# Optimization experiments

Hardware: AMD Instinct MI355X
Metric: run time of the kernel (lower is better)

The kernel has to match this reference:

```python
import jax, jax.numpy as jnp
import numpy as np

B, T, V = 32, 100, 20000
E, H, M, DD = 128, 128, 64, 2


def setup_inputs() -> dict:
    key = jax.random.key(0)
    ks = jax.random.split(key, 12)
    x = jax.random.uniform(ks[0], (B, T, V), dtype=jnp.float32)
    # zero out trailing timesteps per example so Masking layer matters
    lens = jax.random.randint(ks[1], (B,), T * 3 // 4, T + 1)
    tmask = (jnp.arange(T)[None, :] < lens[:, None]).astype(jnp.float32)
    x = x * tmask[:, :, None]
    a = jax.random.uniform(ks[2], (B, V), dtype=jnp.float32)
    d = jax.random.normal(ks[3], (B, DD), dtype=jnp.float32)
    # parameters
    emb = jax.random.uniform(ks[4], (V, E), minval=-0.1, maxval=0.1, dtype=jnp.float32)
    s = 1.0 / np.sqrt(E)
    gru_k = jax.random.uniform(ks[5], (E, 3 * H), minval=-s, maxval=s, dtype=jnp.float32)
    gru_rk = jax.random.normal(ks[6], (H, 3 * H), dtype=jnp.float32) / np.sqrt(H)
    gru_b_i = jnp.zeros((3 * H,), jnp.float32)   # input bias (reset_after=True)
    gru_b_r = jnp.zeros((3 * H,), jnp.float32)   # recurrent bias
    s1 = 1.0 / np.sqrt(H + E)
    W1 = jax.random.uniform(ks[7], (H + E, M), minval=-s1, maxval=s1, dtype=jnp.float32)
    b1 = jnp.zeros((M,), jnp.float32)
    s2 = 1.0 / np.sqrt(M + DD)
    W2 = jax.random.uniform(ks[8], (M + DD, 1), minval=-s2, maxval=s2, dtype=jnp.float32)
    b2 = jnp.zeros((1,), jnp.float32)
    return dict(x=x, a=a, d=d, emb=emb, gru_k=gru_k, gru_rk=gru_rk,
                gru_b_i=gru_b_i, gru_b_r=gru_b_r, W1=W1, b1=b1, W2=W2, b2=b2)


def _gru_final_state(xe, mask, gru_k, gru_rk, gru_b_i, gru_b_r):
    # xe: [B,T,E], mask: [B,T] bool. Keras GRU, reset_after=True, eval mode (dropout off).
    Hn = gru_rk.shape[0]
    x_proj = jnp.einsum('bte,eh->bth', xe, gru_k) + gru_b_i  # [B,T,3H]

    def step(h, inp):
        xp_t, m_t = inp                      # [B,3H], [B]
        rec = h @ gru_rk + gru_b_r           # [B,3H]
        xz, xr, xh = jnp.split(xp_t, 3, axis=-1)
        rz, rr, rh = jnp.split(rec, 3, axis=-1)
        z = jax.nn.sigmoid(xz + rz)
        r = jax.nn.sigmoid(xr + rr)
        hh = jnp.tanh(xh + r * rh)
        h_new = z * h + (1.0 - z) * hh
        h = jnp.where(m_t[:, None], h_new, h)  # masked steps carry state
        return h, None

    h0 = jnp.zeros((xe.shape[0], Hn), xe.dtype)
    h_final, _ = jax.lax.scan(step, h0, (jnp.swapaxes(x_proj, 0, 1), jnp.swapaxes(mask, 0, 1)))
    return h_final


def reference(x, a, d, emb, gru_k, gru_rk, gru_b_i, gru_b_r, W1, b1, W2, b2):
    ae = jnp.tanh(a @ emb)                       # [B,E]
    xe = jnp.tanh(jnp.einsum('btv,ve->bte', x, emb))  # [B,T,E]
    mask = jnp.any(xe != 0.0, axis=-1)           # Masking(mask_value=0.0)
    h = _gru_final_state(xe, mask, gru_k, gru_rk, gru_b_i, gru_b_r)  # [B,H]
    c = jnp.tanh(jnp.concatenate([h, ae], axis=1) @ W1 + b1)         # [B,M]
    out = jax.nn.sigmoid(jnp.concatenate([c, d], axis=1) @ W2 + b2)  # [B,1]
    return out
```

## Files before the change

### kernel.cpp

```cpp
#include <hip/hip_runtime.h>

typedef __attribute__((ext_vector_type(8))) short short8;
typedef __attribute__((ext_vector_type(4))) float float4v;

#define V_ 20000
#define KS 8
#define MPAD 3328

__device__ __forceinline__ unsigned short f2bf(float f) {
    union { float f; unsigned int u; } v; v.f = f;
    unsigned int u = v.u;
    u += 0x7fffu + ((u >> 16) & 1u);
    return (unsigned short)(u >> 16);
}

__device__ __forceinline__ float fast_tanh(float x) {
    float xc = fminf(15.f, fmaxf(-15.f, x));
    float e = __expf(2.f * xc);
    return (e - 1.f) / (e + 1.f);
}

__device__ __forceinline__ float sigmoidf_(float x) {
    float xc = fminf(30.f, fmaxf(-30.f, x));
    return 1.f / (1.f + __expf(-xc));
}

__global__ __launch_bounds__(256) void cvt_embT(const float* __restrict__ emb,
                                                unsigned short* __restrict__ embT) {
    __shared__ unsigned short tile[128 * 65];
    int tid = threadIdx.x;
    int k0 = blockIdx.x * 64;
    const float4v* e4 = (const float4v*)emb;
    #pragma unroll
    for (int c = 0; c < 8; ++c) {
        int l4 = c * 256 + tid;
        int k = l4 >> 5;
        int n4 = l4 & 31;
        float4v f = {0.f, 0.f, 0.f, 0.f};
        if (k0 + k < V_) f = e4[(size_t)(k0 + k) * 32 + n4];
        tile[(n4 * 4 + 0) * 65 + k] = f2bf(f.x);
        tile[(n4 * 4 + 1) * 65 + k] = f2bf(f.y);
        tile[(n4 * 4 + 2) * 65 + k] = f2bf(f.z);
        tile[(n4 * 4 + 3) * 65 + k] = f2bf(f.w);
    }
    __syncthreads();
    #pragma unroll
    for (int c = 0; c < 4; ++c) {
        int l8 = c * 256 + tid;
        int n = l8 >> 3, seg = l8 & 7;
        int kk = k0 + seg * 8;
        if (kk < V_) {
            short8 v;
            #pragma unroll
            for (int i = 0; i < 8; ++i) v[i] = (short)tile[n * 65 + seg * 8 + i];
            *(short8*)(embT + (size_t)n * V_ + kk) = v;
        }
    }
}

__global__ __launch_bounds__(256) void big_gemm(const float* __restrict__ x,
                                                const float* __restrict__ a,
                                                const unsigned short* __restrict__ embT,
                                                float* __restrict__ partial) {
    __shared__ unsigned short Alds[128 * 40];
    __shared__ unsigned short Blds[128 * 40];
    int tid = threadIdx.x;
    int bx = blockIdx.x, by = blockIdx.y;
    int m0 = bx * 128;
    const int per = 625 / KS, extra = 625 % KS;
    int kb0 = by * per + (by < extra ? by : extra);
    int nkb = per + (by < extra ? 1 : 0);

    int lane = tid & 63, wave = tid >> 6;
    int wr = wave >> 1, wc = wave & 1;
    int ln = lane & 15, quad = lane >> 4;

    float4v acc[4][4];
    #pragma unroll
    for (int i = 0; i < 4; ++i)
        #pragma unroll
        for (int j = 0; j < 4; ++j) acc[i][j] = (float4v){0.f, 0.f, 0.f, 0.f};

    int row = tid >> 1, seg = tid & 1;
    int rg = m0 + row;
    int aidx = rg - 3200; if (aidx < 0) aidx = 0; if (aidx > 31) aidx = 31;
    const float* __restrict__ srcA = (rg < 3200) ? (x + (size_t)rg * V_)
                                                 : (a + (size_t)aidx * V_);
    const unsigned short* __restrict__ srcB = embT + (size_t)row * V_;

    for (int it = 0; it < nkb; ++it) {
        int k0 = (kb0 + it) * 32;
        const float4v* ap = (const float4v*)(srcA + k0 + seg * 16);
        float4v f0 = ap[0], f1 = ap[1], f2 = ap[2], f3 = ap[3];
        short8 w0, w1;
        w0[0]=(short)f2bf(f0.x); w0[1]=(short)f2bf(f0.y); w0[2]=(short)f2bf(f0.z); w0[3]=(short)f2bf(f0.w);
        w0[4]=(short)f2bf(f1.x); w0[5]=(short)f2bf(f1.y); w0[6]=(short)f2bf(f1.z); w0[7]=(short)f2bf(f1.w);
        w1[0]=(short)f2bf(f2.x); w1[1]=(short)f2bf(f2.y); w1[2]=(short)f2bf(f2.z); w1[3]=(short)f2bf(f2.w);
        w1[4]=(short)f2bf(f3.x); w1[5]=(short)f2bf(f3.y); w1[6]=(short)f2bf(f3.z); w1[7]=(short)f2bf(f3.w);
        *(short8*)&Alds[row * 40 + seg * 16]     = w0;
        *(short8*)&Alds[row * 40 + seg * 16 + 8] = w1;
        const short8* bp = (const short8*)(srcB + k0 + seg * 16);
        short8 b0 = bp[0], b1 = bp[1];
        *(short8*)&Blds[row * 40 + seg * 16]     = b0;
        *(short8*)&Blds[row * 40 + seg * 16 + 8] = b1;
        __syncthreads();

        short8 af[4];
        #pragma unroll
        for (int i = 0; i < 4; ++i)
            af[i] = *(const short8*)&Alds[(wr * 64 + i * 16 + ln) * 40 + quad * 8];
        #pragma unroll
        for (int j = 0; j < 4; ++j) {
            short8 bf = *(const short8*)&Blds[(wc * 64 + j * 16 + ln) * 40 + quad * 8];
            #pragma unroll
            for (int i = 0; i < 4; ++i)
                acc[i][j] = __builtin_amdgcn_mfma_f32_16x16x32_bf16(af[i], bf, acc[i][j], 0, 0, 0);
        }
        __syncthreads();
    }

    float* dst = partial + (size_t)by * MPAD * 128;
    #pragma unroll
    for (int i = 0; i < 4; ++i) {
        #pragma unroll
        for (int j = 0; j < 4; ++j) {
            int rowb = m0 + wr * 64 + i * 16 + quad * 4;
            int col = wc * 64 + j * 16 + ln;
            #pragma unroll
            for (int r = 0; r < 4; ++r)
                dst[(size_t)(rowb + r) * 128 + col] = acc[i][j][r];
        }
    }
}

__global__ __launch_bounds__(128) void reduce_tanh(const float* __restrict__ partial,
                                                   float* __restrict__ xe,
                                                   float* __restrict__ ae,
                                                   float* __restrict__ maskg) {
    int row = blockIdx.x;
    int e = threadIdx.x;
    float s = 0.f;
    #pragma unroll
    for (int ks = 0; ks < KS; ++ks)
        s += partial[((size_t)ks * MPAD + row) * 128 + e];
    float v = fast_tanh(s);
    if (row < 3200) {
        xe[(size_t)row * 128 + e] = v;
        __shared__ int any;
        if (e == 0) any = 0;
        __syncthreads();
        if (v != 0.f) any = 1;
        __syncthreads();
        if (e == 0) maskg[row] = any ? 1.f : 0.f;
    } else {
        ae[(row - 3200) * 128 + e] = v;
    }
}

__global__ __launch_bounds__(384) void xproj_kernel(const float* __restrict__ xe,
                                                    const float* __restrict__ gru_k,
                                                    const float* __restrict__ b_i,
                                                    float* __restrict__ xproj) {
    __shared__ float xs[16 * 128];
    int tid = threadIdx.x;
    int row0 = blockIdx.x * 16;
    const float4v* src = (const float4v*)(xe + (size_t)row0 * 128);
    float4v* dstl = (float4v*)xs;
    #pragma unroll
    for (int c = 0; c < 2; ++c) {
        int i4 = c * 384 + tid;
        if (i4 < 512) dstl[i4] = src[i4];
    }
    __syncthreads();
    int j = tid;
    float acc[16];
    #pragma unroll
    for (int r = 0; r < 16; ++r) acc[r] = 0.f;
    float bi = b_i[j];
    for (int k4 = 0; k4 < 32; ++k4) {
        float g0 = gru_k[(k4 * 4 + 0) * 384 + j];
        float g1 = gru_k[(k4 * 4 + 1) * 384 + j];
        float g2 = gru_k[(k4 * 4 + 2) * 384 + j];
        float g3 = gru_k[(k4 * 4 + 3) * 384 + j];
        #pragma unroll
        for (int r = 0; r < 16; ++r) {
            float4v xv = *(const float4v*)&xs[r * 128 + k4 * 4];
            acc[r] = fmaf(xv.x, g0, acc[r]);
            acc[r] = fmaf(xv.y, g1, acc[r]);
            acc[r] = fmaf(xv.z, g2, acc[r]);
            acc[r] = fmaf(xv.w, g3, acc[r]);
        }
    }
    #pragma unroll
    for (int r = 0; r < 16; ++r)
        xproj[(size_t)(row0 + r) * 384 + j] = acc[r] + bi;
}

__global__ __launch_bounds__(384) void gru_kernel(const float* __restrict__ xproj,
                                                  const float* __restrict__ maskg,
                                                  const float* __restrict__ gru_rk,
                                                  const float* __restrict__ b_r,
                                                  float* __restrict__ hout) {
    int b = blockIdx.x;
    int j = threadIdx.x;
    float w[128];
    #pragma unroll
    for (int k = 0; k < 128; ++k) w[k] = gru_rk[k * 384 + j];
    float br = b_r[j];
    __shared__ float4v hs4[32];
    __shared__ float xps[384];
    __shared__ float recs[384];
    float* hs = (float*)hs4;
    float hreg = 0.f;
    if (j < 128) hs[j] = 0.f;
    __syncthreads();
    const float* xp_base = xproj + (size_t)b * 100 * 384;
    const float* mk = maskg + b * 100;
    for (int t = 0; t < 100; ++t) {
        float xp = xp_base[t * 384 + j];
        float s0 = 0.f, s1 = 0.f, s2 = 0.f, s3 = 0.f;
        #pragma unroll
        for (int k4 = 0; k4 < 32; ++k4) {
            float4v hv = hs4[k4];
            s0 = fmaf(hv.x, w[k4 * 4 + 0], s0);
            s1 = fmaf(hv.y, w[k4 * 4 + 1], s1);
            s2 = fmaf(hv.z, w[k4 * 4 + 2], s2);
            s3 = fmaf(hv.w, w[k4 * 4 + 3], s3);
        }
        float rec = br + ((s0 + s1) + (s2 + s3));
        xps[j] = xp;
        recs[j] = rec;
        __syncthreads();
        if (j < 128) {
            float z = sigmoidf_(xps[j] + recs[j]);
            float r = sigmoidf_(xps[128 + j] + recs[128 + j]);
            float hh = fast_tanh(xps[256 + j] + r * recs[256 + j]);
            float hn = z * hreg + (1.f - z) * hh;
            float m = mk[t];
            hreg = (m != 0.f) ? hn : hreg;
            hs[j] = hreg;
        }
        __syncthreads();
    }
    if (j < 128) hout[b * 128 + j] = hreg;
}

__global__ __launch_bounds__(64) void head_kernel(const float* __restrict__ hout,
                                                  const float* __restrict__ ae,
                                                  const float* __restrict__ d,
                                                  const float* __restrict__ W1,
                                                  const float* __restrict__ b1,
                                                  const float* __restrict__ W2,
                                                  const float* __restrict__ b2,
                                                  float* __restrict__ out) {
    int b = blockIdx.x;
    int m = threadIdx.x;
    float s = b1[m];
    const float* hb = hout + b * 128;
    const float* ab = ae + b * 128;
    #pragma unroll 4
    for (int k = 0; k < 128; ++k) s = fmaf(hb[k], W1[k * 64 + m], s);
    #pragma unroll 4
    for (int k = 0; k < 128; ++k) s = fmaf(ab[k], W1[(128 + k) * 64 + m], s);
    float c = fast_tanh(s);
    float p = c * W2[m];
    #pragma unroll
    for (int off = 32; off > 0; off >>= 1) p += __shfl_down(p, off);
    if (m == 0) {
        p += d[b * 2 + 0] * W2[64] + d[b * 2 + 1] * W2[65] + b2[0];
        out[b] = sigmoidf_(p);
    }
}

extern "C" void kernel_launch(void* const* d_in, const int* in_sizes, int n_in,
                              void* d_out, int out_size, void* d_ws, size_t ws_size,
                              hipStream_t stream) {
    (void)in_sizes; (void)n_in; (void)out_size; (void)ws_size;
    const float* x      = (const float*)d_in[0];
    const float* a      = (const float*)d_in[1];
    const float* d      = (const float*)d_in[2];
    const float* emb    = (const float*)d_in[3];
    const float* gru_k  = (const float*)d_in[4];
    const float* gru_rk = (const float*)d_in[5];
    const float* gbi    = (const float*)d_in[6];
    const float* gbr    = (const float*)d_in[7];
    const float* W1     = (const float*)d_in[8];
    const float* b1     = (const float*)d_in[9];
    const float* W2     = (const float*)d_in[10];
    const float* b2     = (const float*)d_in[11];
    float* out = (float*)d_out;

    char* ws = (char*)d_ws;
    unsigned short* embT = (unsigned short*)(ws);
    float* partial = (float*)(ws + 5120000);
    float* xe      = (float*)(ws + 18751488);
    float* ae      = (float*)(ws + 20389888);
    float* maskg   = (float*)(ws + 20406272);
    float* xproj   = (float*)(ws + 20419072);
    float* hout    = (float*)(ws + 25334272);

    hipLaunchKernelGGL(cvt_embT,    dim3(313),    dim3(256), 0, stream, emb, embT);
    hipLaunchKernelGGL(big_gemm,    dim3(26, KS), dim3(256), 0, stream, x, a, embT, partial);
    hipLaunchKernelGGL(reduce_tanh, dim3(3232),   dim3(128), 0, stream, partial, xe, ae, maskg);
    hipLaunchKernelGGL(xproj_kernel,dim3(200),    dim3(384), 0, stream, xe, gru_k, gbi, xproj);
    hipLaunchKernelGGL(gru_kernel,  dim3(32),     dim3(384), 0, stream, xproj, maskg, gru_rk, gbr, hout);
    hipLaunchKernelGGL(head_kernel, dim3(32),     dim3(64),  0, stream, hout, ae, d, W1, b1, W2, b2, out);
}
```

Measured before the change: 595.0 us.

## Double-buffer GEMM with direct-to-LDS loads, adaptive split-K, prefetch GRU inputs

The big bf16 GEMM now double-buffers its LDS tiles, prefetching the next K block of A into registers and B via global_load_lds while the MFMAs for the current block run. It also removes one barrier per iteration. The split-K count is now picked at runtime from the workspace size, up to 32, to put more blocks on the GPU; this costs more partial-sum traffic in the reduce kernel. The GRU kernel prefetches the next timestep's input projections into registers and drops the shared xps staging. The global_load_lds layout without padding may cause LDS bank conflicts on the B reads.

```diff
diff --git a/kernel.cpp b/kernel.cpp
--- a/kernel.cpp
+++ b/kernel.cpp
@@ -4,8 +4,6 @@
 typedef __attribute__((ext_vector_type(4))) float float4v;
 
 #define V_ 20000
-#define KS 8
-#define MPAD 3328
 
 __device__ __forceinline__ unsigned short f2bf(float f) {
     union { float f; unsigned int u; } v; v.f = f;
@@ -24,6 +22,10 @@
     float xc = fminf(30.f, fmaxf(-30.f, x));
     return 1.f / (1.f + __expf(-xc));
 }
+
+#define GLL16(gp, lp) __builtin_amdgcn_global_load_lds( \
+    (const __attribute__((address_space(1))) void*)(gp), \
+    (__attribute__((address_space(3))) void*)(lp), 16, 0, 0)
 
 __global__ __launch_bounds__(256) void cvt_embT(const float* __restrict__ emb,
                                                 unsigned short* __restrict__ embT) {
@@ -58,16 +60,17 @@
     }
 }
 
-__global__ __launch_bounds__(256) void big_gemm(const float* __restrict__ x,
-                                                const float* __restrict__ a,
-                                                const unsigned short* __restrict__ embT,
-                                                float* __restrict__ partial) {
-    __shared__ unsigned short Alds[128 * 40];
-    __shared__ unsigned short Blds[128 * 40];
+__global__ __launch_bounds__(256, 4) void big_gemm(const float* __restrict__ x,
+                                                   const float* __restrict__ a,
+                                                   const unsigned short* __restrict__ embT,
+                                                   float* __restrict__ partial,
+                                                   int ks) {
+    __shared__ unsigned short Alds[2][128 * 40];
+    __shared__ unsigned short Blds[2][128 * 32];
     int tid = threadIdx.x;
     int bx = blockIdx.x, by = blockIdx.y;
     int m0 = bx * 128;
-    const int per = 625 / KS, extra = 625 % KS;
+    int per = 625 / ks, extra = 625 % ks;
     int kb0 = by * per + (by < extra ? by : extra);
     int nkb = per + (by < extra ? 1 : 0);
 
@@ -83,43 +86,66 @@
 
     int row = tid >> 1, seg = tid & 1;
     int rg = m0 + row;
-    int aidx = rg - 3200; if (aidx < 0) aidx = 0; if (aidx > 31) aidx = 31;
+    int aidx = rg - 3200; aidx = aidx < 0 ? 0 : (aidx > 31 ? 31 : aidx);
     const float* __restrict__ srcA = (rg < 3200) ? (x + (size_t)rg * V_)
                                                  : (a + (size_t)aidx * V_);
-    const unsigned short* __restrict__ srcB = embT + (size_t)row * V_;
+    int brow0 = tid >> 2, bkq = tid & 3;
+    int wbase = tid & ~63;
+    const unsigned short* gB0 = embT + (size_t)brow0 * V_ + bkq * 8;
+    const unsigned short* gB1 = embT + (size_t)(64 + brow0) * V_ + bkq * 8;
+
+    float4v fa0, fa1, fa2, fa3;
+
+    {
+        int k0 = kb0 * 32;
+        const float4v* ap = (const float4v*)(srcA + k0 + seg * 16);
+        fa0 = ap[0]; fa1 = ap[1]; fa2 = ap[2]; fa3 = ap[3];
+        GLL16(gB0 + k0, &Blds[0][(size_t)wbase * 8]);
+        GLL16(gB1 + k0, &Blds[0][(size_t)(256 + wbase) * 8]);
+        short8 w0, w1;
+        w0[0]=(short)f2bf(fa0.x); w0[1]=(short)f2bf(fa0.y); w0[2]=(short)f2bf(fa0.z); w0[3]=(short)f2bf(fa0.w);
+        w0[4]=(short)f2bf(fa1.x); w0[5]=(short)f2bf(fa1.y); w0[6]=(short)f2bf(fa1.z); w0[7]=(short)f2bf(fa1.w);
+        w1[0]=(short)f2bf(fa2.x); w1[1]=(short)f2bf(fa2.y); w1[2]=(short)f2bf(fa2.z); w1[3]=(short)f2bf(fa2.w);
+        w1[4]=(short)f2bf(fa3.x); w1[5]=(short)f2bf(fa3.y); w1[6]=(short)f2bf(fa3.z); w1[7]=(short)f2bf(fa3.w);
+        *(short8*)&Alds[0][row * 40 + seg * 16]     = w0;
+        *(short8*)&Alds[0][row * 40 + seg * 16 + 8] = w1;
+    }
+    __syncthreads();
 
     for (int it = 0; it < nkb; ++it) {
-        int k0 = (kb0 + it) * 32;
-        const float4v* ap = (const float4v*)(srcA + k0 + seg * 16);
-        float4v f0 = ap[0], f1 = ap[1], f2 = ap[2], f3 = ap[3];
-        short8 w0, w1;
-        w0[0]=(short)f2bf(f0.x); w0[1]=(short)f2bf(f0.y); w0[2]=(short)f2bf(f0.z); w0[3]=(short)f2bf(f0.w);
-        w0[4]=(short)f2bf(f1.x); w0[5]=(short)f2bf(f1.y); w0[6]=(short)f2bf(f1.z); w0[7]=(short)f2bf(f1.w);
-        w1[0]=(short)f2bf(f2.x); w1[1]=(short)f2bf(f2.y); w1[2]=(short)f2bf(f2.z); w1[3]=(short)f2bf(f2.w);
-        w1[4]=(short)f2bf(f3.x); w1[5]=(short)f2bf(f3.y); w1[6]=(short)f2bf(f3.z); w1[7]=(short)f2bf(f3.w);
-        *(short8*)&Alds[row * 40 + seg * 16]     = w0;
-        *(short8*)&Alds[row * 40 + seg * 16 + 8] = w1;
-        const short8* bp = (const short8*)(srcB + k0 + seg * 16);
-        short8 b0 = bp[0], b1 = bp[1];
-        *(short8*)&Blds[row * 40 + seg * 16]     = b0;
-        *(short8*)&Blds[row * 40 + seg * 16 + 8] = b1;
-        __syncthreads();
-
+        int buf = it & 1, nxt = buf ^ 1;
+        bool more = (it + 1 < nkb);
+        if (more) {
+            int k0 = (kb0 + it + 1) * 32;
+            const float4v* ap = (const float4v*)(srcA + k0 + seg * 16);
+            fa0 = ap[0]; fa1 = ap[1]; fa2 = ap[2]; fa3 = ap[3];
+            GLL16(gB0 + k0, &Blds[nxt][(size_t)wbase * 8]);
+            GLL16(gB1 + k0, &Blds[nxt][(size_t)(256 + wbase) * 8]);
+        }
         short8 af[4];
         #pragma unroll
         for (int i = 0; i < 4; ++i)
-            af[i] = *(const short8*)&Alds[(wr * 64 + i * 16 + ln) * 40 + quad * 8];
+            af[i] = *(const short8*)&Alds[buf][(wr * 64 + i * 16 + ln) * 40 + quad * 8];
         #pragma unroll
         for (int j = 0; j < 4; ++j) {
-            short8 bf = *(const short8*)&Blds[(wc * 64 + j * 16 + ln) * 40 + quad * 8];
+            short8 bf = *(const short8*)&Blds[buf][(wc * 64 + j * 16 + ln) * 32 + quad * 8];
             #pragma unroll
             for (int i = 0; i < 4; ++i)
                 acc[i][j] = __builtin_amdgcn_mfma_f32_16x16x32_bf16(af[i], bf, acc[i][j], 0, 0, 0);
         }
-        __syncthreads();
-    }
-
-    float* dst = partial + (size_t)by * MPAD * 128;
+        if (more) {
+            short8 w0, w1;
+            w0[0]=(short)f2bf(fa0.x); w0[1]=(short)f2bf(fa0.y); w0[2]=(short)f2bf(fa0.z); w0[3]=(short)f2bf(fa0.w);
+            w0[4]=(short)f2bf(fa1.x); w0[5]=(short)f2bf(fa1.y); w0[6]=(short)f2bf(fa1.z); w0[7]=(short)f2bf(fa1.w);
+            w1[0]=(short)f2bf(fa2.x); w1[1]=(short)f2bf(fa2.y); w1[2]=(short)f2bf(fa2.z); w1[3]=(short)f2bf(fa2.w);
+            w1[4]=(short)f2bf(fa3.x); w1[5]=(short)f2bf(fa3.y); w1[6]=(short)f2bf(fa3.z); w1[7]=(short)f2bf(fa3.w);
+            *(short8*)&Alds[nxt][row * 40 + seg * 16]     = w0;
+            *(short8*)&Alds[nxt][row * 40 + seg * 16 + 8] = w1;
+        }
+        __syncthreads();
+    }
+
+    float* dst = partial + (size_t)by * 3328 * 128;
     #pragma unroll
     for (int i = 0; i < 4; ++i) {
         #pragma unroll
@@ -136,13 +162,13 @@
 __global__ __launch_bounds__(128) void reduce_tanh(const float* __restrict__ partial,
                                                    float* __restrict__ xe,
                                                    float* __restrict__ ae,
-                                                   float* __restrict__ maskg) {
+                                                   float* __restrict__ maskg,
+                                                   int ks) {
     int row = blockIdx.x;
     int e = threadIdx.x;
     float s = 0.f;
-    #pragma unroll
-    for (int ks = 0; ks < KS; ++ks)
-        s += partial[((size_t)ks * MPAD + row) * 128 + e];
+    for (int k = 0; k < ks; ++k)
+        s += partial[((size_t)k * 3328 + row) * 128 + e];
     float v = fast_tanh(s);
     if (row < 3200) {
         xe[(size_t)row * 128 + e] = v;
@@ -208,16 +234,21 @@
     for (int k = 0; k < 128; ++k) w[k] = gru_rk[k * 384 + j];
     float br = b_r[j];
     __shared__ float4v hs4[32];
-    __shared__ float xps[384];
     __shared__ float recs[384];
     float* hs = (float*)hs4;
     float hreg = 0.f;
     if (j < 128) hs[j] = 0.f;
-    __syncthreads();
     const float* xp_base = xproj + (size_t)b * 100 * 384;
     const float* mk = maskg + b * 100;
+    float xz = 0.f, xr = 0.f, xh = 0.f;
+    if (j < 128) { xz = xp_base[j]; xr = xp_base[128 + j]; xh = xp_base[256 + j]; }
+    __syncthreads();
     for (int t = 0; t < 100; ++t) {
-        float xp = xp_base[t * 384 + j];
+        float nxz = 0.f, nxr = 0.f, nxh = 0.f;
+        if (t < 99 && j < 128) {
+            const float* nb = xp_base + (t + 1) * 384;
+            nxz = nb[j]; nxr = nb[128 + j]; nxh = nb[256 + j];
+        }
         float s0 = 0.f, s1 = 0.f, s2 = 0.f, s3 = 0.f;
         #pragma unroll
         for (int k4 = 0; k4 < 32; ++k4) {
@@ -227,20 +258,18 @@
             s2 = fmaf(hv.z, w[k4 * 4 + 2], s2);
             s3 = fmaf(hv.w, w[k4 * 4 + 3], s3);
         }
-        float rec = br + ((s0 + s1) + (s2 + s3));
-        xps[j] = xp;
-        recs[j] = rec;
+        recs[j] = br + ((s0 + s1) + (s2 + s3));
         __syncthreads();
         if (j < 128) {
-            float z = sigmoidf_(xps[j] + recs[j]);
-            float r = sigmoidf_(xps[128 + j] + recs[128 + j]);
-            float hh = fast_tanh(xps[256 + j] + r * recs[256 + j]);
+            float z = sigmoidf_(xz + recs[j]);
+            float r = sigmoidf_(xr + recs[128 + j]);
+            float hh = fast_tanh(xh + r * recs[256 + j]);
             float hn = z * hreg + (1.f - z) * hh;
-            float m = mk[t];
-            hreg = (m != 0.f) ? hn : hreg;
+            hreg = (mk[t] != 0.f) ? hn : hreg;
             hs[j] = hreg;
         }
         __syncthreads();
+        xz = nxz; xr = nxr; xh = nxh;
     }
     if (j < 128) hout[b * 128 + j] = hreg;
 }
@@ -275,7 +304,7 @@
 extern "C" void kernel_launch(void* const* d_in, const int* in_sizes, int n_in,
                               void* d_out, int out_size, void* d_ws, size_t ws_size,
                               hipStream_t stream) {
-    (void)in_sizes; (void)n_in; (void)out_size; (void)ws_size;
+    (void)in_sizes; (void)n_in; (void)out_size;
     const float* x      = (const float*)d_in[0];
     const float* a      = (const float*)d_in[1];
     const float* d      = (const float*)d_in[2];
@@ -292,17 +321,26 @@
 
     char* ws = (char*)d_ws;
     unsigned short* embT = (unsigned short*)(ws);
-    float* partial = (float*)(ws + 5120000);
-    float* xe      = (float*)(ws + 18751488);
-    float* ae      = (float*)(ws + 20389888);
-    float* maskg   = (float*)(ws + 20406272);
-    float* xproj   = (float*)(ws + 20419072);
-    float* hout    = (float*)(ws + 25334272);
-
-    hipLaunchKernelGGL(cvt_embT,    dim3(313),    dim3(256), 0, stream, emb, embT);
-    hipLaunchKernelGGL(big_gemm,    dim3(26, KS), dim3(256), 0, stream, x, a, embT, partial);
-    hipLaunchKernelGGL(reduce_tanh, dim3(3232),   dim3(128), 0, stream, partial, xe, ae, maskg);
-    hipLaunchKernelGGL(xproj_kernel,dim3(200),    dim3(384), 0, stream, xe, gru_k, gbi, xproj);
-    hipLaunchKernelGGL(gru_kernel,  dim3(32),     dim3(384), 0, stream, xproj, maskg, gru_rk, gbr, hout);
-    hipLaunchKernelGGL(head_kernel, dim3(32),     dim3(64),  0, stream, hout, ae, d, W1, b1, W2, b2, out);
-}
+    float* xe      = (float*)(ws + 5120000);
+    float* ae      = (float*)(ws + 6758400);
+    float* maskg   = (float*)(ws + 6774784);
+    float* xproj   = (float*)(ws + 6787584);
+    float* hout    = (float*)(ws + 11702784);
+    const size_t fixed = 11719168;
+    const size_t slice = (size_t)3328 * 128 * 4;
+    float* partial = (float*)(ws + fixed);
+
+    int ks = 8;
+    if (ws_size > fixed + slice) {
+        size_t avail = (ws_size - fixed) / slice;
+        ks = (int)(avail < 32 ? avail : 32);
+        if (ks < 1) ks = 1;
+    }
+
+    hipLaunchKernelGGL(cvt_embT,    dim3(313),     dim3(256), 0, stream, emb, embT);
+    hipLaunchKernelGGL(big_gemm,    dim3(26, ks),  dim3(256), 0, stream, x, a, embT, partial, ks);
+    hipLaunchKernelGGL(reduce_tanh, dim3(3232),    dim3(128), 0, stream, partial, xe, ae, maskg, ks);
+    hipLaunchKernelGGL(xproj_kernel,dim3(200),     dim3(384), 0, stream, xe, gru_k, gbi, xproj);
+    hipLaunchKernelGGL(gru_kernel,  dim3(32),      dim3(384), 0, stream, xproj, maskg, gru_rk, gbr, hout);
+    hipLaunchKernelGGL(head_kernel, dim3(32),      dim3(64),  0, stream, hout, ae, d, W1, b1, W2, b2, out);
+}
```

Result: faster. 573.5 us (-3.6%).
